# Kernel optimization log

Measured on AMD Instinct MI355X. Metric: run time of the kernel, lower is better.

The kernel has to match this reference:

```python
import jax, jax.numpy as jnp
import numpy as np

STATE_DIM = 256
ACT_LEN = 128
INPUT_DIM = STATE_DIM + 2 * ACT_LEN
B_SZ, T = 32, 2048
SLOPE = 0.01


def leaky(x):
    return jnp.where(x < 0, SLOPE * x, x)


def inv_leaky(x):
    return jnp.where(x < 0, x / SLOPE, x)


def _lin_init(key, out_d, in_d):
    k1, k2 = jax.random.split(key)
    bound = 1.0 / np.sqrt(in_d)
    W = jax.random.uniform(k1, (out_d, in_d), minval=-bound, maxval=bound, dtype=jnp.float32)
    b = jax.random.uniform(k2, (out_d,), minval=-bound, maxval=bound, dtype=jnp.float32)
    return W, b


def setup_inputs() -> dict:
    key = jax.random.key(0)
    ks = jax.random.split(key, 8)
    padded_input = jax.random.normal(ks[0], (B_SZ, T, INPUT_DIM), dtype=jnp.float32)
    We1, be1 = _lin_init(ks[1], STATE_DIM, STATE_DIM)
    We2, be2 = _lin_init(ks[2], STATE_DIM, STATE_DIM)
    A_W, A_b = _lin_init(ks[3], STATE_DIM, STATE_DIM)
    B_W, B_b = _lin_init(ks[4], STATE_DIM, ACT_LEN)
    Wd1, bd1 = _lin_init(ks[5], STATE_DIM, STATE_DIM)
    Wd2, bd2 = _lin_init(ks[6], STATE_DIM, STATE_DIM)
    return {"padded_input": padded_input, "We1": We1, "be1": be1, "We2": We2, "be2": be2,
            "A_W": A_W, "A_b": A_b, "B_W": B_W, "B_b": B_b,
            "Wd1": Wd1, "bd1": bd1, "Wd2": Wd2, "bd2": bd2}


def reference(padded_input, We1, be1, We2, be2, A_W, A_b, B_W, B_b, Wd1, bd1, Wd2, bd2):
    x_t = padded_input[:, :, :STATE_DIM]                      # [B,T,D]
    u_t = padded_input[:, :, STATE_DIM:STATE_DIM + ACT_LEN]   # [B,T,A]
    # encoder: (Linear + LeakyReLU) x 2
    z = leaky(jnp.einsum('btd,ed->bte', x_t, We1) + be1)
    z = leaky(jnp.einsum('btd,ed->bte', z, We2) + be2)
    # recurrence z_{t} uses encoded state only at t=0 (reset_probability=0, nwarmup=0)
    Bu = jnp.einsum('bta,da->btd', u_t, B_W) + B_b            # [B,T,D], precomputed
    z0 = z[:, 0, :]                                           # [B,D]

    def step(carry, bu_t):
        out = jnp.einsum('bd,ed->be', carry, A_W) + A_b + bu_t
        return out, out

    _, z1 = jax.lax.scan(step, z0, jnp.swapaxes(Bu, 0, 1))    # z1: [T,B,D]
    z1 = jnp.swapaxes(z1, 0, 1)                               # [B,T,D]
    # decoder: (InverseLeakyReLU + Linear) x 2
    y = jnp.einsum('btd,ed->bte', inv_leaky(z1), Wd1) + bd1
    y = jnp.einsum('btd,ed->bte', inv_leaky(y), Wd2) + bd2
    return y
```

## Files before the change

### kernel.cpp

```cpp
#include <hip/hip_runtime.h>

#define D256 256
#define ALEN 128
#define INDIM 512
#define BSZ 32
#define TLEN 2048
#define CHL 32
#define NCH 64

typedef __attribute__((ext_vector_type(8))) short short8;
typedef __attribute__((ext_vector_type(4))) float f32x4;

__device__ __forceinline__ float leakyf(float x)  { return x < 0.f ? 0.01f * x : x; }
__device__ __forceinline__ float ileakyf(float x) { return x < 0.f ? x * 100.0f : x; }

__device__ __forceinline__ unsigned short f2bf(float f) {
  unsigned int x = __float_as_uint(f);
  unsigned int r = x + 0x7FFFu + ((x >> 16) & 1u);
  return (unsigned short)(r >> 16);
}

__device__ __forceinline__ void gload16(const void* g, const void* l) {
  __builtin_amdgcn_global_load_lds(
      (const __attribute__((address_space(1))) unsigned int*)g,
      (__attribute__((address_space(3))) unsigned int*)l, 16, 0, 0);
}

template <int CTRL>
__device__ __forceinline__ float dpp_addf(float x) {
  return x + __int_as_float(__builtin_amdgcn_update_dpp(
                 0, __float_as_int(x), CTRL, 0xF, 0xF, true));
}
__device__ __forceinline__ void red8(float4& s) {
  s.x = dpp_addf<0xB1>(s.x); s.y = dpp_addf<0xB1>(s.y);
  s.z = dpp_addf<0xB1>(s.z); s.w = dpp_addf<0xB1>(s.w);
  s.x = dpp_addf<0x4E>(s.x); s.y = dpp_addf<0x4E>(s.y);
  s.z = dpp_addf<0x4E>(s.z); s.w = dpp_addf<0x4E>(s.w);
  s.x = dpp_addf<0x141>(s.x); s.y = dpp_addf<0x141>(s.y);
  s.z = dpp_addf<0x141>(s.z); s.w = dpp_addf<0x141>(s.w);
}

__global__ __launch_bounds__(256) void gemm_mfma(
    const unsigned short* __restrict__ In, int K,
    const unsigned short* __restrict__ W,
    const float* __restrict__ bias1, const float* __restrict__ bias2,
    int ileaky_act, int out_bf16, void* __restrict__ Outp) {
  __shared__ char lds[16384];
  const int tid = threadIdx.x;
  const int lane = tid & 63, w = tid >> 6;
  const int m0 = blockIdx.x * 128, n0 = blockIdx.y * 128;
  const int wm = (w & 1) * 64, wn = (w >> 1) * 64;
  const int quad = lane >> 4, l16 = lane & 15;

  f32x4 acc[4][4];
#pragma unroll
  for (int i = 0; i < 4; ++i)
#pragma unroll
    for (int j = 0; j < 4; ++j) acc[i][j] = {0.f, 0.f, 0.f, 0.f};

  for (int kb = 0; kb < K; kb += 32) {
    __syncthreads();
#pragma unroll
    for (int q = 0; q < 2; ++q) {
      const int id = (w * 2 + q) * 64 + lane;
      const int row = id >> 2, ch = id & 3;
      gload16(In + (size_t)(m0 + row) * K + kb + ch * 8,
              lds + (w * 2 + q) * 1024);
      gload16(W + (size_t)(n0 + row) * K + kb + ch * 8,
              lds + 8192 + (w * 2 + q) * 1024);
    }
    __syncthreads();

    short8 af[4], bf[4];
#pragma unroll
    for (int i = 0; i < 4; ++i) {
      af[i] = *(const short8*)(lds + ((wm + i * 16 + l16) * 64 + quad * 16));
      bf[i] = *(const short8*)(lds + 8192 + ((wn + i * 16 + l16) * 64 + quad * 16));
    }
#pragma unroll
    for (int i = 0; i < 4; ++i)
#pragma unroll
      for (int j = 0; j < 4; ++j)
        acc[i][j] = __builtin_amdgcn_mfma_f32_16x16x32_bf16(af[i], bf[j], acc[i][j], 0, 0, 0);
  }

#pragma unroll
  for (int j = 0; j < 4; ++j) {
    const int n = n0 + wn + j * 16 + l16;
    const float bv = (bias1 ? bias1[n] : 0.f) + (bias2 ? bias2[n] : 0.f);
#pragma unroll
    for (int i = 0; i < 4; ++i) {
#pragma unroll
      for (int r = 0; r < 4; ++r) {
        const int m = m0 + wm + i * 16 + quad * 4 + r;
        float v = acc[i][j][r] + bv;
        if (ileaky_act) v = ileakyf(v);
        if (out_bf16)
          ((unsigned short*)Outp)[(size_t)m * 256 + n] = f2bf(v);
        else
          ((float*)Outp)[(size_t)m * 256 + n] = v;
      }
    }
  }
}

__global__ __launch_bounds__(256) void gemm_sq(
    const float* __restrict__ X, const float* __restrict__ XT,
    float* __restrict__ Out, float* __restrict__ OutT) {
  __shared__ float a_lds[64][40];
  __shared__ float b_lds[64][40];
  const int tid = threadIdx.x;
  const int tm = tid >> 4, tn = tid & 15;
  const int m0 = blockIdx.x * 64, n0 = blockIdx.y * 64;
  float acc[4][4];
#pragma unroll
  for (int i = 0; i < 4; ++i)
#pragma unroll
    for (int j = 0; j < 4; ++j) acc[i][j] = 0.f;

  for (int kb = 0; kb < 256; kb += 32) {
    __syncthreads();
#pragma unroll
    for (int q = 0; q < 2; ++q) {
      const int slot = q * 256 + tid;
      const int row = slot >> 3, s4 = slot & 7;
      *(float4*)&a_lds[row][s4 * 4] = *(const float4*)&X[(size_t)(m0 + row) * 256 + kb + s4 * 4];
      *(float4*)&b_lds[row][s4 * 4] = *(const float4*)&XT[(size_t)(n0 + row) * 256 + kb + s4 * 4];
    }
    __syncthreads();
#pragma unroll
    for (int k4 = 0; k4 < 8; ++k4) {
      float4 a4[4], b4[4];
#pragma unroll
      for (int i = 0; i < 4; ++i) a4[i] = *(const float4*)&a_lds[tm * 4 + i][k4 * 4];
#pragma unroll
      for (int j = 0; j < 4; ++j) b4[j] = *(const float4*)&b_lds[tn * 4 + j][k4 * 4];
#pragma unroll
      for (int i = 0; i < 4; ++i)
#pragma unroll
        for (int j = 0; j < 4; ++j)
          acc[i][j] += a4[i].x * b4[j].x + a4[i].y * b4[j].y +
                       a4[i].z * b4[j].z + a4[i].w * b4[j].w;
    }
  }
#pragma unroll
  for (int i = 0; i < 4; ++i) {
    const int m = m0 + tm * 4 + i;
    *(float4*)&Out[(size_t)m * 256 + n0 + tn * 4] =
        make_float4(acc[i][0], acc[i][1], acc[i][2], acc[i][3]);
#pragma unroll
    for (int j = 0; j < 4; ++j)
      OutT[(size_t)(n0 + tn * 4 + j) * 256 + m] = acc[i][j];
  }
}

__global__ __launch_bounds__(256) void prep_kernel(
    const float* __restrict__ in, const float* __restrict__ We1,
    const float* __restrict__ be1, const float* __restrict__ We2,
    const float* __restrict__ be2, const float* __restrict__ A_W,
    const float* __restrict__ B_W, const float* __restrict__ Wd1,
    const float* __restrict__ Wd2, float* __restrict__ AT,
    float* __restrict__ z0, unsigned short* __restrict__ BWb,
    unsigned short* __restrict__ Wd1b, unsigned short* __restrict__ Wd2b) {
  __shared__ float sm[1056];
  const int tid = threadIdx.x;
  const int blk = blockIdx.x;
  if (blk < 64) {
    const int bx = (blk & 7) * 32, by = (blk >> 3) * 32;
    const int lx = tid & 31, ly = tid >> 5;
#pragma unroll
    for (int i = 0; i < 4; ++i)
      sm[(ly + 8 * i) * 33 + lx] = A_W[(size_t)(by + ly + 8 * i) * 256 + bx + lx];
    __syncthreads();
#pragma unroll
    for (int i = 0; i < 4; ++i)
      AT[(size_t)(bx + ly + 8 * i) * 256 + by + lx] = sm[lx * 33 + ly + 8 * i];
  } else if (blk < 96) {
    const int b = blk - 64, e = tid;
    float* xb = sm;
    float* h1 = sm + 256;
    xb[e] = in[(size_t)b * TLEN * INDIM + e];
    __syncthreads();
    float acc = be1[e];
    const float4* w = (const float4*)(We1 + (size_t)e * 256);
#pragma unroll 8
    for (int d4 = 0; d4 < 64; ++d4) {
      float4 wv = w[d4];
      acc += wv.x * xb[4 * d4] + wv.y * xb[4 * d4 + 1] + wv.z * xb[4 * d4 + 2] + wv.w * xb[4 * d4 + 3];
    }
    h1[e] = leakyf(acc);
    __syncthreads();
    float a2 = be2[e];
    w = (const float4*)(We2 + (size_t)e * 256);
#pragma unroll 8
    for (int d4 = 0; d4 < 64; ++d4) {
      float4 wv = w[d4];
      a2 += wv.x * h1[4 * d4] + wv.y * h1[4 * d4 + 1] + wv.z * h1[4 * d4 + 2] + wv.w * h1[4 * d4 + 3];
    }
    z0[(size_t)b * 256 + e] = leakyf(a2);
  } else {
    const float* src;
    unsigned short* dst;
    int i4;
    if (blk < 128)      { src = B_W; dst = BWb;  i4 = (blk - 96) * 256 + tid; }
    else if (blk < 192) { src = Wd1; dst = Wd1b; i4 = (blk - 128) * 256 + tid; }
    else                { src = Wd2; dst = Wd2b; i4 = (blk - 192) * 256 + tid; }
    float4 v = *(const float4*)&src[(size_t)i4 * 4];
    *(ushort4*)&dst[(size_t)i4 * 4] =
        make_ushort4(f2bf(v.x), f2bf(v.y), f2bf(v.z), f2bf(v.w));
  }
}

__global__ __launch_bounds__(256) void extract_u(const float* __restrict__ in,
                                                 unsigned short* __restrict__ ubuf) {
  const int gid = blockIdx.x * 256 + threadIdx.x;
  const int row = gid >> 5;
  const int c = (gid & 31) * 4;
  float4 v = *(const float4*)&in[(size_t)row * INDIM + 256 + c];
  *(ushort4*)&ubuf[(size_t)row * 128 + c] =
      make_ushort4(f2bf(v.x), f2bf(v.y), f2bf(v.z), f2bf(v.w));
}

__global__ __launch_bounds__(512, 2) void phase_kernel(
    const float* __restrict__ AW, const float* __restrict__ Cbuf,
    const float* __restrict__ Einit, float* __restrict__ Lend,
    unsigned short* __restrict__ w1out) {
  const int tid = threadIdx.x;
  const int w = tid >> 6;
  const int lane = tid & 63;
  const int dg = lane & 7;
  const int le = lane >> 3;
  const int e0 = w * 32 + le * 4;
  const int d0 = dg * 32;
  const int rho0 = blockIdx.x << 3;
  const int k = rho0 >> 5;
  const int b = (rho0 & 31) + dg;
  const int rho = rho0 + dg;

  __shared__ __align__(16) float carry[2][8][292];

  float4 Ar[4][8];
#pragma unroll
  for (int i = 0; i < 4; ++i)
#pragma unroll
    for (int k4 = 0; k4 < 8; ++k4)
      Ar[i][k4] = *(const float4*)&AW[(size_t)(e0 + i) * 256 + d0 + k4 * 4];

  float4 cur;
  if (Einit) cur = *(const float4*)&Einit[(size_t)rho * 256 + e0];
  else       cur = make_float4(0.f, 0.f, 0.f, 0.f);
  const int epad = e0 + ((e0 >> 5) << 2);
  *(float4*)&carry[0][dg][epad] = cur;
  __syncthreads();

  const float4* crow = (const float4*)(Cbuf + ((size_t)b * TLEN + (size_t)k * CHL) * 256 + e0);
  ushort4* wrow = w1out
      ? (ushort4*)(w1out + ((size_t)b * TLEN + (size_t)k * CHL) * 256 + e0)
      : (ushort4*)0;

  int buf = 0;
  for (int j = 0; j < CHL; ++j) {
    float4 cj = *crow;
    crow += 64;
    float4 nxt = make_float4(0.f, 0.f, 0.f, 0.f);
#pragma unroll
    for (int r = 0; r < 8; ++r) {
      float4 s = make_float4(0.f, 0.f, 0.f, 0.f);
#pragma unroll
      for (int k4 = 0; k4 < 8; ++k4) {
        const float4 cv = *(const float4*)&carry[buf][r][dg * 36 + k4 * 4];
        s.x += Ar[0][k4].x * cv.x + Ar[0][k4].y * cv.y + Ar[0][k4].z * cv.z + Ar[0][k4].w * cv.w;
        s.y += Ar[1][k4].x * cv.x + Ar[1][k4].y * cv.y + Ar[1][k4].z * cv.z + Ar[1][k4].w * cv.w;
        s.z += Ar[2][k4].x * cv.x + Ar[2][k4].y * cv.y + Ar[2][k4].z * cv.z + Ar[2][k4].w * cv.w;
        s.w += Ar[3][k4].x * cv.x + Ar[3][k4].y * cv.y + Ar[3][k4].z * cv.z + Ar[3][k4].w * cv.w;
      }
      red8(s);
      if (dg == r) nxt = s;
    }
    cur = make_float4(nxt.x + cj.x, nxt.y + cj.y, nxt.z + cj.z, nxt.w + cj.w);
    buf ^= 1;
    *(float4*)&carry[buf][dg][epad] = cur;
    if (w1out) {
      *wrow = make_ushort4(f2bf(ileakyf(cur.x)), f2bf(ileakyf(cur.y)),
                           f2bf(ileakyf(cur.z)), f2bf(ileakyf(cur.w)));
      wrow += 64;
    }
    __syncthreads();
  }
  if (Lend) *(float4*)&Lend[(size_t)rho * 256 + e0] = cur;
}

__global__ __launch_bounds__(512, 2) void boundary_kernel(
    const float* __restrict__ P, const float* __restrict__ z0,
    const float* __restrict__ Lend, float* __restrict__ Earr) {
  const int tid = threadIdx.x;
  const int w = tid >> 6;
  const int lane = tid & 63;
  const int dg = lane & 7;
  const int le = lane >> 3;
  const int e0 = w * 32 + le * 4;
  const int d0 = dg * 32;
  const int b = blockIdx.x;

  __shared__ __align__(16) float Ec[292];

  float4 Pr[4][8];
#pragma unroll
  for (int i = 0; i < 4; ++i)
#pragma unroll
    for (int k4 = 0; k4 < 8; ++k4)
      Pr[i][k4] = *(const float4*)&P[(size_t)(e0 + i) * 256 + d0 + k4 * 4];

  float4 cur = *(const float4*)&z0[(size_t)b * 256 + e0];
  const int epad = e0 + ((e0 >> 5) << 2);
  if (dg == 0) *(float4*)&Ec[epad] = cur;
  __syncthreads();

  for (int k = 0; k < NCH; ++k) {
    const float4 lv = *(const float4*)&Lend[((size_t)k * BSZ + b) * 256 + e0];
    if (dg == 0) *(float4*)&Earr[((size_t)k * BSZ + b) * 256 + e0] = cur;

    float4 s = make_float4(0.f, 0.f, 0.f, 0.f);
#pragma unroll
    for (int k4 = 0; k4 < 8; ++k4) {
      const float4 cv = *(const float4*)&Ec[dg * 36 + k4 * 4];
      s.x += Pr[0][k4].x * cv.x + Pr[0][k4].y * cv.y + Pr[0][k4].z * cv.z + Pr[0][k4].w * cv.w;
      s.y += Pr[1][k4].x * cv.x + Pr[1][k4].y * cv.y + Pr[1][k4].z * cv.z + Pr[1][k4].w * cv.w;
      s.z += Pr[2][k4].x * cv.x + Pr[2][k4].y * cv.y + Pr[2][k4].z * cv.z + Pr[2][k4].w * cv.w;
      s.w += Pr[3][k4].x * cv.x + Pr[3][k4].y * cv.y + Pr[3][k4].z * cv.z + Pr[3][k4].w * cv.w;
    }
    red8(s);
    cur = make_float4(s.x + lv.x, s.y + lv.y, s.z + lv.z, s.w + lv.w);
    __syncthreads();
    if (dg == 0) *(float4*)&Ec[epad] = cur;
    __syncthreads();
  }
}

extern "C" void kernel_launch(void* const* d_in, const int* in_sizes, int n_in,
                              void* d_out, int out_size, void* d_ws, size_t ws_size,
                              hipStream_t stream) {
  const float* in  = (const float*)d_in[0];
  const float* We1 = (const float*)d_in[1];
  const float* be1 = (const float*)d_in[2];
  const float* We2 = (const float*)d_in[3];
  const float* be2 = (const float*)d_in[4];
  const float* A_W = (const float*)d_in[5];
  const float* A_b = (const float*)d_in[6];
  const float* B_W = (const float*)d_in[7];
  const float* B_b = (const float*)d_in[8];
  const float* Wd1 = (const float*)d_in[9];
  const float* bd1 = (const float*)d_in[10];
  const float* Wd2 = (const float*)d_in[11];
  const float* bd2 = (const float*)d_in[12];
  float* out = (float*)d_out;

  float* ws   = (float*)d_ws;
  float* Cbuf = ws;
  float* AT   = Cbuf + 16777216;
  float* PT   = AT + 65536;
  float* Pa   = PT + 65536;
  float* PaT  = Pa + 65536;
  float* Pb   = PaT + 65536;
  float* PbT  = Pb + 65536;
  float* z0   = PbT + 65536;
  float* Lend = z0 + 8192;
  float* Earr = Lend + 524288;
  unsigned short* BWb  = (unsigned short*)(Earr + 524288);
  unsigned short* Wd1b = BWb + 32768;
  unsigned short* Wd2b = Wd1b + 65536;

  unsigned short* ubuf = (unsigned short*)d_out;
  unsigned short* w1   = ubuf + 8388608;
  unsigned short* w2   = (unsigned short*)Cbuf;

  prep_kernel<<<256, 256, 0, stream>>>(in, We1, be1, We2, be2, A_W, B_W, Wd1,
                                       Wd2, AT, z0, BWb, Wd1b, Wd2b);
  extract_u<<<8192, 256, 0, stream>>>(in, ubuf);

  gemm_mfma<<<dim3(512, 2), 256, 0, stream>>>(ubuf, ALEN, BWb, A_b, B_b, 0, 0, Cbuf);

  gemm_sq<<<dim3(4, 4), 256, 0, stream>>>(A_W, AT, Pa, PaT);
  gemm_sq<<<dim3(4, 4), 256, 0, stream>>>(Pa, PaT, Pb, PbT);
  gemm_sq<<<dim3(4, 4), 256, 0, stream>>>(Pb, PbT, Pa, PaT);
  gemm_sq<<<dim3(4, 4), 256, 0, stream>>>(Pa, PaT, Pb, PbT);
  gemm_sq<<<dim3(4, 4), 256, 0, stream>>>(Pb, PbT, Pa, PT);

  phase_kernel<<<256, 512, 0, stream>>>(A_W, Cbuf, nullptr, Lend, nullptr);
  boundary_kernel<<<32, 512, 0, stream>>>(Pa, z0, Lend, Earr);
  phase_kernel<<<256, 512, 0, stream>>>(A_W, Cbuf, Earr, nullptr, w1);

  gemm_mfma<<<dim3(512, 2), 256, 0, stream>>>(w1, D256, Wd1b, bd1, nullptr, 1, 1, w2);
  gemm_mfma<<<dim3(512, 2), 256, 0, stream>>>(w2, D256, Wd2b, bd2, nullptr, 0, 0, out);
}
```

Before: 754.9 us.

## Replace second recurrence pass with power-stack correction GEMM on MFMA

New measurement: 757.6 us. No clear change (+0.4%).

```diff
diff --git a/kernel.cpp b/kernel.cpp
--- a/kernel.cpp
+++ b/kernel.cpp
@@ -18,6 +18,10 @@
   unsigned int x = __float_as_uint(f);
   unsigned int r = x + 0x7FFFu + ((x >> 16) & 1u);
   return (unsigned short)(r >> 16);
+}
+
+__device__ __forceinline__ float bf2f(unsigned short u) {
+  return __uint_as_float(((unsigned int)u) << 16);
 }
 
 __device__ __forceinline__ void gload16(const void* g, const void* l) {
@@ -104,11 +108,74 @@
   }
 }
 
-__global__ __launch_bounds__(256) void gemm_sq(
-    const float* __restrict__ X, const float* __restrict__ XT,
-    float* __restrict__ Out, float* __restrict__ OutT) {
+__global__ __launch_bounds__(256) void gemm_corr(
+    const unsigned short* __restrict__ Eb, const unsigned short* __restrict__ Mb,
+    const float* __restrict__ Df, unsigned short* __restrict__ w1) {
+  __shared__ char lds[16384];
+  const int tid = threadIdx.x;
+  const int lane = tid & 63, w = tid >> 6;
+  const int m0 = blockIdx.x * 128, n0 = blockIdx.y * 128;
+  const int wm = (w & 1) * 64, wn = (w >> 1) * 64;
+  const int quad = lane >> 4, l16 = lane & 15;
+
+  f32x4 acc[4][4];
+#pragma unroll
+  for (int i = 0; i < 4; ++i)
+#pragma unroll
+    for (int j = 0; j < 4; ++j) acc[i][j] = {0.f, 0.f, 0.f, 0.f};
+
+  for (int kb = 0; kb < 256; kb += 32) {
+    __syncthreads();
+#pragma unroll
+    for (int q = 0; q < 2; ++q) {
+      const int id = (w * 2 + q) * 64 + lane;
+      const int row = id >> 2, ch = id & 3;
+      gload16(Eb + (size_t)(m0 + row) * 256 + kb + ch * 8,
+              lds + (w * 2 + q) * 1024);
+      gload16(Mb + (size_t)(n0 + row) * 256 + kb + ch * 8,
+              lds + 8192 + (w * 2 + q) * 1024);
+    }
+    __syncthreads();
+
+    short8 af[4], bf[4];
+#pragma unroll
+    for (int i = 0; i < 4; ++i) {
+      af[i] = *(const short8*)(lds + ((wm + i * 16 + l16) * 64 + quad * 16));
+      bf[i] = *(const short8*)(lds + 8192 + ((wn + i * 16 + l16) * 64 + quad * 16));
+    }
+#pragma unroll
+    for (int i = 0; i < 4; ++i)
+#pragma unroll
+      for (int j = 0; j < 4; ++j)
+        acc[i][j] = __builtin_amdgcn_mfma_f32_16x16x32_bf16(af[i], bf[j], acc[i][j], 0, 0, 0);
+  }
+
+#pragma unroll
+  for (int jf = 0; jf < 4; ++jf) {
+    const int n = n0 + wn + jf * 16 + l16;
+    const int jj = n >> 8, e = n & 255;
+#pragma unroll
+    for (int i = 0; i < 4; ++i) {
+#pragma unroll
+      for (int r = 0; r < 4; ++r) {
+        const int m = m0 + wm + i * 16 + quad * 4 + r;
+        const int kk = m >> 5, bb = m & 31;
+        const size_t addr = ((size_t)bb * TLEN + (size_t)kk * CHL + jj) * 256 + e;
+        float v = acc[i][jf][r] + Df[addr];
+        w1[addr] = f2bf(ileakyf(v));
+      }
+    }
+  }
+}
+
+__global__ __launch_bounds__(256) void gemm_pow(
+    const float* __restrict__ P, const float* __restrict__ XTb,
+    float* __restrict__ OutS, float* __restrict__ OutST,
+    unsigned short* __restrict__ OutSb) {
   __shared__ float a_lds[64][40];
   __shared__ float b_lds[64][40];
+  const size_t zo = (size_t)blockIdx.z << 16;
+  const float* XT = XTb + zo;
   const int tid = threadIdx.x;
   const int tm = tid >> 4, tn = tid & 15;
   const int m0 = blockIdx.x * 64, n0 = blockIdx.y * 64;
@@ -124,7 +191,7 @@
     for (int q = 0; q < 2; ++q) {
       const int slot = q * 256 + tid;
       const int row = slot >> 3, s4 = slot & 7;
-      *(float4*)&a_lds[row][s4 * 4] = *(const float4*)&X[(size_t)(m0 + row) * 256 + kb + s4 * 4];
+      *(float4*)&a_lds[row][s4 * 4] = *(const float4*)&P[(size_t)(m0 + row) * 256 + kb + s4 * 4];
       *(float4*)&b_lds[row][s4 * 4] = *(const float4*)&XT[(size_t)(n0 + row) * 256 + kb + s4 * 4];
     }
     __syncthreads();
@@ -143,11 +210,16 @@
                        a4[i].z * b4[j].z + a4[i].w * b4[j].w;
     }
   }
+  float* Out = OutS + zo;
+  float* OutT = OutST + zo;
+  unsigned short* Ob = OutSb + zo;
 #pragma unroll
   for (int i = 0; i < 4; ++i) {
     const int m = m0 + tm * 4 + i;
-    *(float4*)&Out[(size_t)m * 256 + n0 + tn * 4] =
-        make_float4(acc[i][0], acc[i][1], acc[i][2], acc[i][3]);
+    float4 v = make_float4(acc[i][0], acc[i][1], acc[i][2], acc[i][3]);
+    *(float4*)&Out[(size_t)m * 256 + n0 + tn * 4] = v;
+    *(ushort4*)&Ob[(size_t)m * 256 + n0 + tn * 4] =
+        make_ushort4(f2bf(v.x), f2bf(v.y), f2bf(v.z), f2bf(v.w));
 #pragma unroll
     for (int j = 0; j < 4; ++j)
       OutT[(size_t)(n0 + tn * 4 + j) * 256 + m] = acc[i][j];
@@ -159,9 +231,10 @@
     const float* __restrict__ be1, const float* __restrict__ We2,
     const float* __restrict__ be2, const float* __restrict__ A_W,
     const float* __restrict__ B_W, const float* __restrict__ Wd1,
-    const float* __restrict__ Wd2, float* __restrict__ AT,
-    float* __restrict__ z0, unsigned short* __restrict__ BWb,
-    unsigned short* __restrict__ Wd1b, unsigned short* __restrict__ Wd2b) {
+    const float* __restrict__ Wd2, float* __restrict__ AT0,
+    unsigned short* __restrict__ Ab0, float* __restrict__ z0,
+    unsigned short* __restrict__ BWb, unsigned short* __restrict__ Wd1b,
+    unsigned short* __restrict__ Wd2b) {
   __shared__ float sm[1056];
   const int tid = threadIdx.x;
   const int blk = blockIdx.x;
@@ -169,12 +242,15 @@
     const int bx = (blk & 7) * 32, by = (blk >> 3) * 32;
     const int lx = tid & 31, ly = tid >> 5;
 #pragma unroll
+    for (int i = 0; i < 4; ++i) {
+      const float v = A_W[(size_t)(by + ly + 8 * i) * 256 + bx + lx];
+      sm[(ly + 8 * i) * 33 + lx] = v;
+      Ab0[(size_t)(by + ly + 8 * i) * 256 + bx + lx] = f2bf(v);
+    }
+    __syncthreads();
+#pragma unroll
     for (int i = 0; i < 4; ++i)
-      sm[(ly + 8 * i) * 33 + lx] = A_W[(size_t)(by + ly + 8 * i) * 256 + bx + lx];
-    __syncthreads();
-#pragma unroll
-    for (int i = 0; i < 4; ++i)
-      AT[(size_t)(bx + ly + 8 * i) * 256 + by + lx] = sm[lx * 33 + ly + 8 * i];
+      AT0[(size_t)(bx + ly + 8 * i) * 256 + by + lx] = sm[lx * 33 + ly + 8 * i];
   } else if (blk < 96) {
     const int b = blk - 64, e = tid;
     float* xb = sm;
@@ -222,9 +298,8 @@
 }
 
 __global__ __launch_bounds__(512, 2) void phase_kernel(
-    const float* __restrict__ AW, const float* __restrict__ Cbuf,
-    const float* __restrict__ Einit, float* __restrict__ Lend,
-    unsigned short* __restrict__ w1out) {
+    const float* __restrict__ AW, float* __restrict__ Cbuf,
+    float* __restrict__ Lend) {
   const int tid = threadIdx.x;
   const int w = tid >> 6;
   const int lane = tid & 63;
@@ -246,53 +321,50 @@
     for (int k4 = 0; k4 < 8; ++k4)
       Ar[i][k4] = *(const float4*)&AW[(size_t)(e0 + i) * 256 + d0 + k4 * 4];
 
-  float4 cur;
-  if (Einit) cur = *(const float4*)&Einit[(size_t)rho * 256 + e0];
-  else       cur = make_float4(0.f, 0.f, 0.f, 0.f);
+  float4 cur = make_float4(0.f, 0.f, 0.f, 0.f);
   const int epad = e0 + ((e0 >> 5) << 2);
   *(float4*)&carry[0][dg][epad] = cur;
   __syncthreads();
 
-  const float4* crow = (const float4*)(Cbuf + ((size_t)b * TLEN + (size_t)k * CHL) * 256 + e0);
-  ushort4* wrow = w1out
-      ? (ushort4*)(w1out + ((size_t)b * TLEN + (size_t)k * CHL) * 256 + e0)
-      : (ushort4*)0;
+  float4* crow = (float4*)(Cbuf + ((size_t)b * TLEN + (size_t)k * CHL) * 256 + e0);
 
   int buf = 0;
   for (int j = 0; j < CHL; ++j) {
-    float4 cj = *crow;
-    crow += 64;
+    const float4 cj = *crow;
+    float4 s[8];
+#pragma unroll
+    for (int r = 0; r < 8; ++r) s[r] = make_float4(0.f, 0.f, 0.f, 0.f);
+#pragma unroll
+    for (int k4 = 0; k4 < 8; ++k4) {
+      const float4 a0 = Ar[0][k4], a1 = Ar[1][k4], a2 = Ar[2][k4], a3 = Ar[3][k4];
+#pragma unroll
+      for (int r = 0; r < 8; ++r) {
+        const float4 cv = *(const float4*)&carry[buf][r][dg * 36 + k4 * 4];
+        s[r].x += a0.x * cv.x + a0.y * cv.y + a0.z * cv.z + a0.w * cv.w;
+        s[r].y += a1.x * cv.x + a1.y * cv.y + a1.z * cv.z + a1.w * cv.w;
+        s[r].z += a2.x * cv.x + a2.y * cv.y + a2.z * cv.z + a2.w * cv.w;
+        s[r].w += a3.x * cv.x + a3.y * cv.y + a3.z * cv.z + a3.w * cv.w;
+      }
+    }
     float4 nxt = make_float4(0.f, 0.f, 0.f, 0.f);
 #pragma unroll
     for (int r = 0; r < 8; ++r) {
-      float4 s = make_float4(0.f, 0.f, 0.f, 0.f);
-#pragma unroll
-      for (int k4 = 0; k4 < 8; ++k4) {
-        const float4 cv = *(const float4*)&carry[buf][r][dg * 36 + k4 * 4];
-        s.x += Ar[0][k4].x * cv.x + Ar[0][k4].y * cv.y + Ar[0][k4].z * cv.z + Ar[0][k4].w * cv.w;
-        s.y += Ar[1][k4].x * cv.x + Ar[1][k4].y * cv.y + Ar[1][k4].z * cv.z + Ar[1][k4].w * cv.w;
-        s.z += Ar[2][k4].x * cv.x + Ar[2][k4].y * cv.y + Ar[2][k4].z * cv.z + Ar[2][k4].w * cv.w;
-        s.w += Ar[3][k4].x * cv.x + Ar[3][k4].y * cv.y + Ar[3][k4].z * cv.z + Ar[3][k4].w * cv.w;
-      }
-      red8(s);
-      if (dg == r) nxt = s;
+      red8(s[r]);
+      if (dg == r) nxt = s[r];
     }
     cur = make_float4(nxt.x + cj.x, nxt.y + cj.y, nxt.z + cj.z, nxt.w + cj.w);
     buf ^= 1;
     *(float4*)&carry[buf][dg][epad] = cur;
-    if (w1out) {
-      *wrow = make_ushort4(f2bf(ileakyf(cur.x)), f2bf(ileakyf(cur.y)),
-                           f2bf(ileakyf(cur.z)), f2bf(ileakyf(cur.w)));
-      wrow += 64;
-    }
-    __syncthreads();
-  }
-  if (Lend) *(float4*)&Lend[(size_t)rho * 256 + e0] = cur;
+    *crow = cur;
+    crow += 64;
+    __syncthreads();
+  }
+  *(float4*)&Lend[(size_t)rho * 256 + e0] = cur;
 }
 
 __global__ __launch_bounds__(512, 2) void boundary_kernel(
     const float* __restrict__ P, const float* __restrict__ z0,
-    const float* __restrict__ Lend, float* __restrict__ Earr) {
+    const float* __restrict__ Lend, unsigned short* __restrict__ Eb) {
   const int tid = threadIdx.x;
   const int w = tid >> 6;
   const int lane = tid & 63;
@@ -318,7 +390,9 @@
 
   for (int k = 0; k < NCH; ++k) {
     const float4 lv = *(const float4*)&Lend[((size_t)k * BSZ + b) * 256 + e0];
-    if (dg == 0) *(float4*)&Earr[((size_t)k * BSZ + b) * 256 + e0] = cur;
+    if (dg == 0)
+      *(ushort4*)&Eb[((size_t)k * BSZ + b) * 256 + e0] =
+          make_ushort4(f2bf(cur.x), f2bf(cur.y), f2bf(cur.z), f2bf(cur.w));
 
     float4 s = make_float4(0.f, 0.f, 0.f, 0.f);
 #pragma unroll
@@ -355,40 +429,38 @@
   const float* bd2 = (const float*)d_in[12];
   float* out = (float*)d_out;
 
-  float* ws   = (float*)d_ws;
-  float* Cbuf = ws;
-  float* AT   = Cbuf + 16777216;
-  float* PT   = AT + 65536;
-  float* Pa   = PT + 65536;
-  float* PaT  = Pa + 65536;
-  float* Pb   = PaT + 65536;
-  float* PbT  = Pb + 65536;
-  float* z0   = PbT + 65536;
-  float* Lend = z0 + 8192;
-  float* Earr = Lend + 524288;
-  unsigned short* BWb  = (unsigned short*)(Earr + 524288);
+  float* ws     = (float*)d_ws;
+  float* Cbuf   = ws;
+  float* Mstack = Cbuf + 16777216;
+  float* z0     = Mstack + 2097152;
+  float* Lend   = z0 + 8192;
+  unsigned short* Mstackb = (unsigned short*)(Lend + 524288);
+  unsigned short* Eb   = Mstackb + 2097152;
+  unsigned short* BWb  = Eb + 524288;
   unsigned short* Wd1b = BWb + 32768;
   unsigned short* Wd2b = Wd1b + 65536;
+  float* MstackT = Cbuf;
 
   unsigned short* ubuf = (unsigned short*)d_out;
   unsigned short* w1   = ubuf + 8388608;
   unsigned short* w2   = (unsigned short*)Cbuf;
 
   prep_kernel<<<256, 256, 0, stream>>>(in, We1, be1, We2, be2, A_W, B_W, Wd1,
-                                       Wd2, AT, z0, BWb, Wd1b, Wd2b);
+                                       Wd2, MstackT, Mstackb, z0, BWb, Wd1b, Wd2b);
+
+  gemm_pow<<<dim3(4, 4, 1),  256, 0, stream>>>(A_W,                 MstackT, Mstack + 1 * 65536,  MstackT + 1 * 65536,  Mstackb + 1 * 65536);
+  gemm_pow<<<dim3(4, 4, 2),  256, 0, stream>>>(Mstack + 1 * 65536,  MstackT, Mstack + 2 * 65536,  MstackT + 2 * 65536,  Mstackb + 2 * 65536);
+  gemm_pow<<<dim3(4, 4, 4),  256, 0, stream>>>(Mstack + 3 * 65536,  MstackT, Mstack + 4 * 65536,  MstackT + 4 * 65536,  Mstackb + 4 * 65536);
+  gemm_pow<<<dim3(4, 4, 8),  256, 0, stream>>>(Mstack + 7 * 65536,  MstackT, Mstack + 8 * 65536,  MstackT + 8 * 65536,  Mstackb + 8 * 65536);
+  gemm_pow<<<dim3(4, 4, 16), 256, 0, stream>>>(Mstack + 15 * 65536, MstackT, Mstack + 16 * 65536, MstackT + 16 * 65536, Mstackb + 16 * 65536);
+
   extract_u<<<8192, 256, 0, stream>>>(in, ubuf);
 
   gemm_mfma<<<dim3(512, 2), 256, 0, stream>>>(ubuf, ALEN, BWb, A_b, B_b, 0, 0, Cbuf);
 
-  gemm_sq<<<dim3(4, 4), 256, 0, stream>>>(A_W, AT, Pa, PaT);
-  gemm_sq<<<dim3(4, 4), 256, 0, stream>>>(Pa, PaT, Pb, PbT);
-  gemm_sq<<<dim3(4, 4), 256, 0, stream>>>(Pb, PbT, Pa, PaT);
-  gemm_sq<<<dim3(4, 4), 256, 0, stream>>>(Pa, PaT, Pb, PbT);
-  gemm_sq<<<dim3(4, 4), 256, 0, stream>>>(Pb, PbT, Pa, PT);
-
-  phase_kernel<<<256, 512, 0, stream>>>(A_W, Cbuf, nullptr, Lend, nullptr);
-  boundary_kernel<<<32, 512, 0, stream>>>(Pa, z0, Lend, Earr);
-  phase_kernel<<<256, 512, 0, stream>>>(A_W, Cbuf, Earr, nullptr, w1);
+  phase_kernel<<<256, 512, 0, stream>>>(A_W, Cbuf, Lend);
+  boundary_kernel<<<32, 512, 0, stream>>>(Mstack + 31 * 65536, z0, Lend, Eb);
+  gemm_corr<<<dim3(16, 64), 256, 0, stream>>>(Eb, Mstackb, Cbuf, w1);
 
   gemm_mfma<<<dim3(512, 2), 256, 0, stream>>>(w1, D256, Wd1b, bd1, nullptr, 1, 1, w2);
   gemm_mfma<<<dim3(512, 2), 256, 0, stream>>>(w2, D256, Wd2b, bd2, nullptr, 0, 0, out);
```
